# Kernel optimization log

Measured on AMD Instinct MI355X. Metric: run time of the kernel, lower is better.

Reference implementation:

```python
import jax, jax.numpy as jnp
import numpy as np

EPS = 1e-20
TEMP = 0.07
PATCH = 64
STEP = 32  # patch_size * overlap(0.5)


def zero_softmax(x, eps=1e-5):
    # ZeroSoftmax: ((exp(x)-1)^2) / (sum + eps), maps x==0 -> exactly 0 weight
    e = jnp.square(jnp.exp(x) - 1.0)
    return e / (jnp.sum(e, axis=-1, keepdims=True) + eps)


def _scaling_mask(H, W, p, step):
    # constant overlap-count mask from CRW.compute_scaling_mask (static shapes)
    sm = np.zeros((H, W), np.float32)
    for i in range(0, H - step, step):
        for j in range(0, W - step, step):
            sm[i:i + p, j:j + p] += 1.0
    return jnp.asarray(sm)


def _window_sums(m, p, step):
    # m: (B,T,SP,H,W) -> sliding-window sums (B,T,SP,nH,nW) via integral image
    ii = jnp.cumsum(jnp.cumsum(m, axis=-2), axis=-1)
    ii = jnp.pad(ii, ((0, 0), (0, 0), (0, 0), (1, 0), (1, 0)))
    H = m.shape[-2]
    nH = (H - p) // step + 1
    lo = jnp.arange(nH) * step
    hi = lo + p
    r_hi = ii[..., hi, :]   # (B,T,SP,nH,W+1)
    r_lo = ii[..., lo, :]
    return r_hi[..., hi] - r_hi[..., lo] - r_lo[..., hi] + r_lo[..., lo]


def setup_inputs() -> dict:
    key = jax.random.key(0)
    k1, k2, k3 = jax.random.split(key, 3)
    B, T, H, W = 2, 4, 256, 256
    nH = (H - PATCH) // STEP + 1  # 7
    N = nH * nH                   # 49 patches
    Cenc, D, SP = 512, 128, 64
    feats = jax.random.normal(k1, (B, N, Cenc, T), jnp.float32)
    W_head = jax.random.normal(k2, (Cenc, D), jnp.float32) / np.sqrt(Cenc)
    sp_mask = jax.random.randint(k3, (B, T, H, W), 0, SP, jnp.int32)
    return {"feats": feats, "W_head": W_head, "sp_mask": sp_mask, "max_sp_num": SP}


def reference(feats, W_head, sp_mask, max_sp_num):
    B, N, Cenc, T = feats.shape
    H, W = sp_mask.shape[-2:]
    SP = max_sp_num

    # --- pixels_to_nodes tail: projection head + L2 normalize over channel dim ---
    q = jnp.einsum('bnct,cd->bndt', feats, W_head)            # (B,N,128,T)
    nrm = jnp.maximum(jnp.linalg.norm(q, axis=2, keepdims=True), 1e-12)
    q = q / nrm
    q = jnp.transpose(q, (0, 2, 3, 1))                        # (B,128,T,N)

    # --- patches_to_sp_embeddings: windowed superpixel pooling ---
    oh = (sp_mask[:, :, None, :, :] ==
          jnp.arange(SP, dtype=sp_mask.dtype)[None, None, :, None, None]
          ).astype(jnp.float32)                               # (B,T,SP,H,W)
    sm = _scaling_mask(H, W, PATCH, STEP)                     # (H,W)
    ws = _window_sums(oh / sm, PATCH, STEP)                   # (B,T,SP,nH,nW)
    denom = jnp.sum(oh, axis=(-1, -2)) + EPS                  # (B,T,SP)
    wts = jnp.transpose(ws, (0, 1, 3, 4, 2)) / denom[:, :, None, None, :]
    wts = wts.reshape(B, T, N, SP)                            # (B,T,N,SP)
    q_sp = jnp.einsum('bdtn,btns->bdts', q, wts)              # (B,128,T,SP)

    # --- affinity + zero_softmax stochastic matrices ---
    As = jnp.einsum('bdtn,bdtm->btnm', q_sp[:, :, :-1], q_sp[:, :, 1:])  # (B,T-1,SP,SP)
    A12 = zero_softmax(As / TEMP)
    A21 = zero_softmax(jnp.swapaxes(As, -1, -2) / TEMP)

    # --- palindrome random walks + cross-entropy to cycle-consistency targets ---
    tgt = jnp.tile(jnp.arange(SP), B)
    loss = jnp.float32(0.0)
    AAs = []
    for i in range(1, T - 1):
        mats = [A12[:, k] for k in range(i + 1)] + [A21[:, k] for k in range(i, -1, -1)]
        aa = mats[0]
        for m in mats[1:]:
            aa = aa @ m
        AAs.append(aa)
        logits = jnp.log(aa + EPS).reshape(B * SP, SP)
        logp = jax.nn.log_softmax(logits, axis=-1)
        loss = loss + jnp.mean(-logp[jnp.arange(B * SP), tgt])
    return loss, jnp.stack(AAs)
```

## Files before the change

kernel.cpp:

```cpp
#include <hip/hip_runtime.h>
#include <hip/hip_bf16.h>

constexpr int NWIN = 49;
constexpr int QLD  = 52;

constexpr int OFF_WS   = 0;
constexpr int OFF_Q    = 26624;
constexpr int OFF_QSP  = 79872;
constexpr int OFF_A12  = 145408;
constexpr int OFF_A12T = 169984;
constexpr int OFF_A21  = 194560;
constexpr int OFF_A21T = 219136;

__global__ void __launch_bounds__(256, 1)
k_front(const int* __restrict__ mask, const float* __restrict__ feats,
        const float* __restrict__ Wh, float* __restrict__ ws, float* __restrict__ q) {
    if (blockIdx.x < 392) {
        int win = blockIdx.x % NWIN;
        int bt  = blockIdx.x / NWIN;
        int wy = win / 7, wx = win % 7;
        __shared__ float loc[64];
        if (threadIdx.x < 64) loc[threadIdx.x] = 0.f;
        __syncthreads();
        const int* base = mask + bt * 65536 + (wy * 32) * 256 + wx * 32;
        #pragma unroll
        for (int it = 0; it < 16; ++it) {
            int idx = it * 256 + (int)threadIdx.x;
            int r = idx >> 6, c = idx & 63;
            int s = base[r * 256 + c];
            int y = wy * 32 + r, x = wx * 32 + c;
            float w = 1.f;
            if (y >= 32 && y < 224) w *= 0.5f;
            if (x >= 32 && x < 224) w *= 0.5f;
            atomicAdd(&loc[s], w);
        }
        __syncthreads();
        if (threadIdx.x < 64) {
            ws[(bt * 64 + (int)threadIdx.x) * QLD + win] = loc[threadIdx.x];
        } else if (win == 0) {
            int s = threadIdx.x & 63;
            int col = 49 + (int)(threadIdx.x >> 6) - 1;
            ws[(bt * 64 + s) * QLD + col] = 0.f;
        }
    } else {
        int bid = blockIdx.x - 392;
        int n = bid % NWIN, b = bid / NWIN;
        __shared__ float4 f4[512];
        __shared__ float4 psum4[256];
        __shared__ float4 red4[2];
        const float4* fp4 = (const float4*)(feats + (size_t)(b * NWIN + n) * 2048);
        for (int i = threadIdx.x; i < 512; i += 256) f4[i] = fp4[i];
        __syncthreads();

        int d = threadIdx.x & 127, ch = threadIdx.x >> 7;
        float a0 = 0.f, a1 = 0.f, a2 = 0.f, a3 = 0.f;
        const float* wp = Wh + d;
        int c0 = ch * 256;
        #pragma unroll 8
        for (int c = c0; c < c0 + 256; ++c) {
            float w = wp[c * 128];
            float4 fv = f4[c];
            a0 += fv.x * w; a1 += fv.y * w; a2 += fv.z * w; a3 += fv.w * w;
        }
        psum4[threadIdx.x] = make_float4(a0, a1, a2, a3);
        __syncthreads();

        float4 A;
        if (threadIdx.x < 128) {
            float4 p0 = psum4[threadIdx.x], p1 = psum4[128 + threadIdx.x];
            A = make_float4(p0.x + p1.x, p0.y + p1.y, p0.z + p1.z, p0.w + p1.w);
            float sx = A.x * A.x, sy = A.y * A.y, sz = A.z * A.z, sw = A.w * A.w;
            for (int off = 32; off; off >>= 1) {
                sx += __shfl_down(sx, off); sy += __shfl_down(sy, off);
                sz += __shfl_down(sz, off); sw += __shfl_down(sw, off);
            }
            if ((threadIdx.x & 63) == 0) red4[threadIdx.x >> 6] = make_float4(sx, sy, sz, sw);
        }
        __syncthreads();
        if (threadIdx.x < 128) {
            float4 r0 = red4[0], r1 = red4[1];
            float ix = 1.f / fmaxf(sqrtf(r0.x + r1.x), 1e-12f);
            float iy = 1.f / fmaxf(sqrtf(r0.y + r1.y), 1e-12f);
            float iz = 1.f / fmaxf(sqrtf(r0.z + r1.z), 1e-12f);
            float iw = 1.f / fmaxf(sqrtf(r0.w + r1.w), 1e-12f);
            float* qb = q + (size_t)(b * 128 + d) * 4 * QLD + n;
            qb[0 * QLD] = A.x * ix;
            qb[1 * QLD] = A.y * iy;
            qb[2 * QLD] = A.z * iz;
            qb[3 * QLD] = A.w * iw;
        }
    }
}

__global__ void k_qsp(const float* __restrict__ q, const float* __restrict__ wsg,
                      float* __restrict__ qsp) {
    int tid = blockIdx.x * 256 + threadIdx.x;
    int s = tid & 63;
    int d = (tid >> 6) & 127;
    int t = (tid >> 13) & 3;
    int b = tid >> 15;
    const float4* qrow = (const float4*)(q + (size_t)((b * 128 + d) * 4 + t) * QLD);
    const float4* wrow = (const float4*)(wsg + (size_t)((b * 4 + t) * 64 + s) * QLD);
    float acc = 0.f, den = 0.f;
    #pragma unroll
    for (int i = 0; i < 13; ++i) {
        float4 w = wrow[i];
        float4 qv = qrow[i];
        den += w.x + w.y + w.z + w.w;
        acc += qv.x * w.x + qv.y * w.y + qv.z * w.z + qv.w * w.w;
    }
    qsp[tid] = acc / (den + 1e-20f);
}

__global__ void __launch_bounds__(256, 1)
k_as(const float* __restrict__ qsp,
     float* __restrict__ a12, float* __restrict__ a12T,
     float* __restrict__ a21, float* __restrict__ a21T, float* __restrict__ out) {
    int t = blockIdx.x % 3, b = blockIdx.x / 3;
    if (blockIdx.x == 0 && threadIdx.x == 0) out[0] = 0.f;
    __shared__ float4 qaT4[64 * 32];
    __shared__ float4 qbT4[64 * 32];
    const int tid = threadIdx.x;

    {
        const float4* gA = (const float4*)(qsp + (size_t)(b * 4 + t) * 8192);
        const float4* gB = (const float4*)(qsp + (size_t)(b * 4 + t + 1) * 8192);
        float* qaF = (float*)qaT4;
        float* qbF = (float*)qbT4;
        #pragma unroll
        for (int it = 0; it < 8; ++it) {
            int idx = it * 256 + tid;
            int d = idx >> 4, s0 = (idx & 15) << 2;
            float4 va = gA[idx];
            float4 vb = gB[idx];
            int g = d >> 2, c = d & 3;
            #pragma unroll
            for (int u = 0; u < 4; ++u) {
                int s = s0 + u;
                int w = (s * 32 + (g ^ (s & 31))) * 4 + c;
                float fa = (u == 0) ? va.x : (u == 1) ? va.y : (u == 2) ? va.z : va.w;
                float fb = (u == 0) ? vb.x : (u == 1) ? vb.y : (u == 2) ? vb.z : vb.w;
                qaF[w] = fa;
                qbF[w] = fb;
            }
        }
    }
    __syncthreads();

    const int nl = tid >> 4, ml = tid & 15;
    float acc[16];
    #pragma unroll
    for (int i = 0; i < 16; ++i) acc[i] = 0.f;
    #pragma unroll 8
    for (int k4 = 0; k4 < 32; ++k4) {
        float4 av[4], bv[4];
        #pragma unroll
        for (int i = 0; i < 4; ++i) { int n = nl + 16 * i; av[i] = qaT4[n * 32 + (k4 ^ (n & 31))]; }
        #pragma unroll
        for (int j = 0; j < 4; ++j) { int m = ml + 16 * j; bv[j] = qbT4[m * 32 + (k4 ^ (m & 31))]; }
        #pragma unroll
        for (int i = 0; i < 4; ++i)
            #pragma unroll
            for (int j = 0; j < 4; ++j)
                acc[i * 4 + j] += av[i].x * bv[j].x + av[i].y * bv[j].y
                                + av[i].z * bv[j].z + av[i].w * bv[j].w;
    }
    __syncthreads();

    float* eb = (float*)qaT4;
    float* rs = (float*)qbT4;
    float* cs = rs + 64;
    #pragma unroll
    for (int i = 0; i < 4; ++i)
        #pragma unroll
        for (int j = 0; j < 4; ++j) {
            int n = nl + 16 * i, m = ml + 16 * j;
            float x = acc[i * 4 + j] * (1.f / 0.07f);
            float e = expf(x) - 1.f;
            eb[n * 65 + m] = e * e;
        }
    __syncthreads();
    if (tid < 128) {
        int r = tid & 63; bool isrow = tid < 64;
        float a = 0.f;
        #pragma unroll
        for (int k = 0; k < 64; ++k) a += isrow ? eb[r * 65 + k] : eb[k * 65 + r];
        (isrow ? rs : cs)[r] = a + 1e-5f;
    }
    __syncthreads();
    float* p12  = a12  + (b * 3 + t) * 4096;
    float* p12T = a12T + (b * 3 + t) * 4096;
    float* p21  = a21  + (b * 3 + t) * 4096;
    float* p21T = a21T + (b * 3 + t) * 4096;
    #pragma unroll
    for (int i = 0; i < 4; ++i)
        #pragma unroll
        for (int j = 0; j < 4; ++j) {
            int n = nl + 16 * i, m = ml + 16 * j;
            float v   = eb[n * 65 + m];
            float v12 = v / rs[n];
            float v21 = v / cs[m];
            p12 [n * 64 + m] = v12;
            p12T[m * 64 + n] = v12;
            p21 [m * 64 + n] = v21;
            p21T[n * 64 + m] = v21;
        }
}


__device__ __forceinline__ void dump_mat(float* M, const float4* v) {
    #pragma unroll
    for (int it = 0; it < 4; ++it) {
        int idx = it * 256 + (int)threadIdx.x;
        int r = idx >> 4, c4 = (idx & 15) << 2;
        *(float4*)&M[r * 64 + (c4 ^ ((r & 15) << 2))] = v[it];
    }
}

__device__ __forceinline__ void mmh_sw(float* acc, const float* Ra, const float* Rb) {
    int lt = threadIdx.x & 127;
    int nl = lt >> 3, ml = lt & 7;
    int sxa = nl << 2;
    #pragma unroll
    for (int k0 = 0; k0 < 64; k0 += 4) {
        float4 av[4], bv[8];
        #pragma unroll
        for (int i = 0; i < 4; ++i)
            av[i] = *(const float4*)&Ra[(nl + 16 * i) * 64 + (k0 ^ sxa)];
        #pragma unroll
        for (int j = 0; j < 8; ++j) {
            int m = ml + 8 * j;
            bv[j] = *(const float4*)&Rb[m * 64 + (k0 ^ ((m & 15) << 2))];
        }
        #pragma unroll
        for (int i = 0; i < 4; ++i)
            #pragma unroll
            for (int j = 0; j < 8; ++j)
                acc[i * 8 + j] += av[i].x * bv[j].x + av[i].y * bv[j].y
                                + av[i].z * bv[j].z + av[i].w * bv[j].w;
    }
}

__device__ __forceinline__ void wrh_sw(float* M, const float* acc) {
    int lt = threadIdx.x & 127;
    int nl = lt >> 3, ml = lt & 7;
    #pragma unroll
    for (int i = 0; i < 4; ++i)
        #pragma unroll
        for (int j = 0; j < 8; ++j) {
            int r = nl + 16 * i, k = ml + 8 * j;
            M[r * 64 + (((k & ~3) ^ ((r & 15) << 2)) | (k & 3))] = acc[i * 8 + j];
        }
}

__device__ __forceinline__ void mm256_sw(float* acc, const float* Ra, const float* Rb) {
    int tid = threadIdx.x;
    int nl = tid >> 4, ml = tid & 15;
    int sxa = nl << 2, sxb = ml << 2;
    #pragma unroll
    for (int i = 0; i < 16; ++i) acc[i] = 0.f;
    #pragma unroll 4
    for (int k0 = 0; k0 < 64; k0 += 4) {
        float4 av[4], bv[4];
        #pragma unroll
        for (int i = 0; i < 4; ++i)
            av[i] = *(const float4*)&Ra[(nl + 16 * i) * 64 + (k0 ^ sxa)];
        #pragma unroll
        for (int j = 0; j < 4; ++j)
            bv[j] = *(const float4*)&Rb[(ml + 16 * j) * 64 + (k0 ^ sxb)];
        #pragma unroll
        for (int i = 0; i < 4; ++i)
            #pragma unroll
            for (int j = 0; j < 4; ++j)
                acc[i * 4 + j] += av[i].x * bv[j].x + av[i].y * bv[j].y
                                + av[i].z * bv[j].z + av[i].w * bv[j].w;
    }
}

__device__ __forceinline__ void store_loss(const float* acc, float* __restrict__ aa,
                                           float* __restrict__ out, float* red) {
    int tid = threadIdx.x;
    int nl = tid >> 4, ml = tid & 15;
    #pragma unroll
    for (int i = 0; i < 4; ++i)
        #pragma unroll
        for (int j = 0; j < 4; ++j)
            aa[(nl + 16 * i) * 64 + (ml + 16 * j)] = acc[i * 4 + j];
    int l = tid & 63;
    float part = 0.f;
    #pragma unroll
    for (int i = 0; i < 4; ++i) {
        float rsum = acc[i * 4 + 0] + acc[i * 4 + 1] + acc[i * 4 + 2] + acc[i * 4 + 3];
        rsum += __shfl_down(rsum, 8, 16);
        rsum += __shfl_down(rsum, 4, 16);
        rsum += __shfl_down(rsum, 2, 16);
        rsum += __shfl_down(rsum, 1, 16);
        float dv = __shfl(acc[5 * i], (l & 48) | nl, 64);
        if ((l & 15) == 0) part += logf(rsum + 6.4e-19f) - logf(dv + 1e-20f);
    }
    for (int off = 32; off; off >>= 1) part += __shfl_down(part, off);
    if (l == 0) red[tid >> 6] = part;
    __syncthreads();
    if (tid == 0) atomicAdd(out, (red[0] + red[1] + red[2] + red[3]) * (1.f / 128.f));
}

__global__ void __launch_bounds__(256, 1)
k_chain(const float* __restrict__ a12, const float* __restrict__ a12T,
        const float* __restrict__ a21, const float* __restrict__ a21T,
        float* __restrict__ out) {
    int path = blockIdx.x & 1, b = blockIdx.x >> 1;
    __shared__ float M[4 * 4096];
    float* M0 = M;
    float* M1 = M + 4096;
    float* M2 = M + 8192;
    float* M3 = M + 12288;
    const int tid = threadIdx.x;

    const float4* L0 = (const float4*)(a12  + (b * 3 + 0) * 4096);
    const float4* L1 = (const float4*)(a12T + (b * 3 + 1) * 4096);
    const float4* L2 = (const float4*)(a21T + (b * 3 + 0) * 4096);
    const float4* L3 = (const float4*)(a21  + (b * 3 + 1) * 4096);
    const float4* L4 = (const float4*)(a12T + (b * 3 + 2) * 4096);
    const float4* L5 = (const float4*)(a21  + (b * 3 + 2) * 4096);

    float4 pf[6][4];
    #pragma unroll
    for (int it = 0; it < 4; ++it) {
        int idx = it * 256 + tid;
        pf[0][it] = L0[idx];
        pf[1][it] = L1[idx];
        pf[2][it] = L2[idx];
        pf[3][it] = L3[idx];
    }
    if (path) {
        #pragma unroll
        for (int it = 0; it < 4; ++it) {
            int idx = it * 256 + tid;
            pf[4][it] = L4[idx];
            pf[5][it] = L5[idx];
        }
    }
    dump_mat(M0, pf[0]);
    dump_mat(M1, pf[1]);
    dump_mat(M2, pf[2]);
    dump_mat(M3, pf[3]);
    __syncthreads();

    int half = tid >> 7;
    float hacc[32];
    #pragma unroll
    for (int i = 0; i < 32; ++i) hacc[i] = 0.f;
    mmh_sw(hacc, half ? M2 : M0, half ? M3 : M1);
    __syncthreads();
    wrh_sw(half ? M3 : M1, hacc);
    if (path) { dump_mat(M0, pf[4]); dump_mat(M2, pf[5]); }
    __syncthreads();

    if (path == 0) {
        float acc[16];
        mm256_sw(acc, M1, M3);
        store_loss(acc, out + 1 + b * 4096, out, M0);
    } else {
        float hacc2[32];
        #pragma unroll
        for (int i = 0; i < 32; ++i) hacc2[i] = 0.f;
        mmh_sw(hacc2, half ? M3 : M1, half ? M2 : M0);
        __syncthreads();
        wrh_sw(half ? M1 : M0, hacc2);
        __syncthreads();
        float acc[16];
        mm256_sw(acc, M0, M1);
        store_loss(acc, out + 1 + (2 + b) * 4096, out, M2);
    }
}

extern "C" void kernel_launch(void* const* d_in, const int* in_sizes, int n_in,
                              void* d_out, int out_size, void* d_ws, size_t ws_size,
                              hipStream_t stream) {
    const float* feats = (const float*)d_in[0];
    const float* Wh    = (const float*)d_in[1];
    const int*   mask  = (const int*)d_in[2];
    float* out = (float*)d_out;
    float* ws  = (float*)d_ws;

    float* ws_sums = ws + OFF_WS;
    float* q       = ws + OFF_Q;
    float* qsp     = ws + OFF_QSP;
    float* a12     = ws + OFF_A12;
    float* a12T    = ws + OFF_A12T;
    float* a21     = ws + OFF_A21;
    float* a21T    = ws + OFF_A21T;

    k_front<<<392 + 2 * NWIN, 256, 0, stream>>>(mask, feats, Wh, ws_sums, q);
    k_qsp<<<256, 256, 0, stream>>>(q, ws_sums, qsp);
    k_as<<<6, 256, 0, stream>>>(qsp, a12, a12T, a21, a21T, out);
    k_chain<<<4, 256, 0, stream>>>(a12, a12T, a21, a21T, out);
}
```

Before: 118.9 us.

## Fuse affinity and chain kernels into one persistent kernel with grid barriers

```diff
diff --git a/kernel.cpp b/kernel.cpp
--- a/kernel.cpp
+++ b/kernel.cpp
@@ -11,6 +11,11 @@
 constexpr int OFF_A12T = 169984;
 constexpr int OFF_A21  = 194560;
 constexpr int OFF_A21T = 219136;
+constexpr int OFF_P    = 243712;
+constexpr int OFF_R1T  = 251904;
+constexpr int OFF_L    = 260096;
+constexpr int OFF_RT   = 268288;
+constexpr int OFF_BAR  = 276480;
 
 __global__ void __launch_bounds__(256, 1)
 k_front(const int* __restrict__ mask, const float* __restrict__ feats,
@@ -93,7 +98,12 @@
 }
 
 __global__ void k_qsp(const float* __restrict__ q, const float* __restrict__ wsg,
-                      float* __restrict__ qsp) {
+                      float* __restrict__ qsp, float* __restrict__ out,
+                      int* __restrict__ bar) {
+    if (blockIdx.x == 0 && threadIdx.x < 4) {
+        bar[threadIdx.x] = 0;
+        if (threadIdx.x == 0) out[0] = 0.f;
+    }
     int tid = blockIdx.x * 256 + threadIdx.x;
     int s = tid & 63;
     int d = (tid >> 6) & 127;
@@ -112,101 +122,6 @@
     qsp[tid] = acc / (den + 1e-20f);
 }
 
-__global__ void __launch_bounds__(256, 1)
-k_as(const float* __restrict__ qsp,
-     float* __restrict__ a12, float* __restrict__ a12T,
-     float* __restrict__ a21, float* __restrict__ a21T, float* __restrict__ out) {
-    int t = blockIdx.x % 3, b = blockIdx.x / 3;
-    if (blockIdx.x == 0 && threadIdx.x == 0) out[0] = 0.f;
-    __shared__ float4 qaT4[64 * 32];
-    __shared__ float4 qbT4[64 * 32];
-    const int tid = threadIdx.x;
-
-    {
-        const float4* gA = (const float4*)(qsp + (size_t)(b * 4 + t) * 8192);
-        const float4* gB = (const float4*)(qsp + (size_t)(b * 4 + t + 1) * 8192);
-        float* qaF = (float*)qaT4;
-        float* qbF = (float*)qbT4;
-        #pragma unroll
-        for (int it = 0; it < 8; ++it) {
-            int idx = it * 256 + tid;
-            int d = idx >> 4, s0 = (idx & 15) << 2;
-            float4 va = gA[idx];
-            float4 vb = gB[idx];
-            int g = d >> 2, c = d & 3;
-            #pragma unroll
-            for (int u = 0; u < 4; ++u) {
-                int s = s0 + u;
-                int w = (s * 32 + (g ^ (s & 31))) * 4 + c;
-                float fa = (u == 0) ? va.x : (u == 1) ? va.y : (u == 2) ? va.z : va.w;
-                float fb = (u == 0) ? vb.x : (u == 1) ? vb.y : (u == 2) ? vb.z : vb.w;
-                qaF[w] = fa;
-                qbF[w] = fb;
-            }
-        }
-    }
-    __syncthreads();
-
-    const int nl = tid >> 4, ml = tid & 15;
-    float acc[16];
-    #pragma unroll
-    for (int i = 0; i < 16; ++i) acc[i] = 0.f;
-    #pragma unroll 8
-    for (int k4 = 0; k4 < 32; ++k4) {
-        float4 av[4], bv[4];
-        #pragma unroll
-        for (int i = 0; i < 4; ++i) { int n = nl + 16 * i; av[i] = qaT4[n * 32 + (k4 ^ (n & 31))]; }
-        #pragma unroll
-        for (int j = 0; j < 4; ++j) { int m = ml + 16 * j; bv[j] = qbT4[m * 32 + (k4 ^ (m & 31))]; }
-        #pragma unroll
-        for (int i = 0; i < 4; ++i)
-            #pragma unroll
-            for (int j = 0; j < 4; ++j)
-                acc[i * 4 + j] += av[i].x * bv[j].x + av[i].y * bv[j].y
-                                + av[i].z * bv[j].z + av[i].w * bv[j].w;
-    }
-    __syncthreads();
-
-    float* eb = (float*)qaT4;
-    float* rs = (float*)qbT4;
-    float* cs = rs + 64;
-    #pragma unroll
-    for (int i = 0; i < 4; ++i)
-        #pragma unroll
-        for (int j = 0; j < 4; ++j) {
-            int n = nl + 16 * i, m = ml + 16 * j;
-            float x = acc[i * 4 + j] * (1.f / 0.07f);
-            float e = expf(x) - 1.f;
-            eb[n * 65 + m] = e * e;
-        }
-    __syncthreads();
-    if (tid < 128) {
-        int r = tid & 63; bool isrow = tid < 64;
-        float a = 0.f;
-        #pragma unroll
-        for (int k = 0; k < 64; ++k) a += isrow ? eb[r * 65 + k] : eb[k * 65 + r];
-        (isrow ? rs : cs)[r] = a + 1e-5f;
-    }
-    __syncthreads();
-    float* p12  = a12  + (b * 3 + t) * 4096;
-    float* p12T = a12T + (b * 3 + t) * 4096;
-    float* p21  = a21  + (b * 3 + t) * 4096;
-    float* p21T = a21T + (b * 3 + t) * 4096;
-    #pragma unroll
-    for (int i = 0; i < 4; ++i)
-        #pragma unroll
-        for (int j = 0; j < 4; ++j) {
-            int n = nl + 16 * i, m = ml + 16 * j;
-            float v   = eb[n * 65 + m];
-            float v12 = v / rs[n];
-            float v21 = v / cs[m];
-            p12 [n * 64 + m] = v12;
-            p12T[m * 64 + n] = v12;
-            p21 [m * 64 + n] = v21;
-            p21T[n * 64 + m] = v21;
-        }
-}
-
 
 __device__ __forceinline__ void dump_mat(float* M, const float4* v) {
     #pragma unroll
@@ -217,40 +132,20 @@
     }
 }
 
-__device__ __forceinline__ void mmh_sw(float* acc, const float* Ra, const float* Rb) {
-    int lt = threadIdx.x & 127;
-    int nl = lt >> 3, ml = lt & 7;
-    int sxa = nl << 2;
-    #pragma unroll
-    for (int k0 = 0; k0 < 64; k0 += 4) {
-        float4 av[4], bv[8];
-        #pragma unroll
-        for (int i = 0; i < 4; ++i)
-            av[i] = *(const float4*)&Ra[(nl + 16 * i) * 64 + (k0 ^ sxa)];
-        #pragma unroll
-        for (int j = 0; j < 8; ++j) {
-            int m = ml + 8 * j;
-            bv[j] = *(const float4*)&Rb[m * 64 + (k0 ^ ((m & 15) << 2))];
-        }
-        #pragma unroll
-        for (int i = 0; i < 4; ++i)
-            #pragma unroll
-            for (int j = 0; j < 8; ++j)
-                acc[i * 8 + j] += av[i].x * bv[j].x + av[i].y * bv[j].y
-                                + av[i].z * bv[j].z + av[i].w * bv[j].w;
-    }
-}
-
-__device__ __forceinline__ void wrh_sw(float* M, const float* acc) {
-    int lt = threadIdx.x & 127;
-    int nl = lt >> 3, ml = lt & 7;
-    #pragma unroll
-    for (int i = 0; i < 4; ++i)
-        #pragma unroll
-        for (int j = 0; j < 8; ++j) {
-            int r = nl + 16 * i, k = ml + 8 * j;
-            M[r * 64 + (((k & ~3) ^ ((r & 15) << 2)) | (k & 3))] = acc[i * 8 + j];
-        }
+__device__ __forceinline__ void stage2(float* Ma, float* Mb,
+                                       const float* __restrict__ Ga,
+                                       const float* __restrict__ Gb) {
+    const float4* ga = (const float4*)Ga;
+    const float4* gb = (const float4*)Gb;
+    float4 va[4], vb[4];
+    #pragma unroll
+    for (int it = 0; it < 4; ++it) {
+        int idx = it * 256 + (int)threadIdx.x;
+        va[it] = ga[idx];
+        vb[it] = gb[idx];
+    }
+    dump_mat(Ma, va);
+    dump_mat(Mb, vb);
 }
 
 __device__ __forceinline__ void mm256_sw(float* acc, const float* Ra, const float* Rb) {
@@ -275,6 +170,15 @@
                 acc[i * 4 + j] += av[i].x * bv[j].x + av[i].y * bv[j].y
                                 + av[i].z * bv[j].z + av[i].w * bv[j].w;
     }
+}
+
+__device__ __forceinline__ void store_mat(float* __restrict__ G, const float* acc) {
+    int nl = threadIdx.x >> 4, ml = threadIdx.x & 15;
+    #pragma unroll
+    for (int i = 0; i < 4; ++i)
+        #pragma unroll
+        for (int j = 0; j < 4; ++j)
+            G[(nl + 16 * i) * 64 + ml + 16 * j] = acc[i * 4 + j];
 }
 
 __device__ __forceinline__ void store_loss(const float* acc, float* __restrict__ aa,
@@ -304,73 +208,174 @@
     if (tid == 0) atomicAdd(out, (red[0] + red[1] + red[2] + red[3]) * (1.f / 128.f));
 }
 
+__device__ __forceinline__ void gbar(int* cnt, int target) {
+    __threadfence();
+    __syncthreads();
+    if (threadIdx.x == 0) {
+        __hip_atomic_fetch_add(cnt, 1, __ATOMIC_ACQ_REL, __HIP_MEMORY_SCOPE_AGENT);
+        while (__hip_atomic_load(cnt, __ATOMIC_ACQUIRE, __HIP_MEMORY_SCOPE_AGENT) < target)
+            __builtin_amdgcn_s_sleep(2);
+    }
+    __syncthreads();
+    __threadfence();
+}
+
 __global__ void __launch_bounds__(256, 1)
-k_chain(const float* __restrict__ a12, const float* __restrict__ a12T,
-        const float* __restrict__ a21, const float* __restrict__ a21T,
-        float* __restrict__ out) {
-    int path = blockIdx.x & 1, b = blockIdx.x >> 1;
-    __shared__ float M[4 * 4096];
-    float* M0 = M;
-    float* M1 = M + 4096;
-    float* M2 = M + 8192;
-    float* M3 = M + 12288;
+k_tail(const float* __restrict__ qsp,
+       float* __restrict__ a12, float* __restrict__ a12T,
+       float* __restrict__ a21, float* __restrict__ a21T,
+       float* __restrict__ wsP, float* __restrict__ wsR1T,
+       float* __restrict__ wsL, float* __restrict__ wsRT,
+       float* __restrict__ out, int* __restrict__ bar) {
+    __shared__ float SM[16384];
     const int tid = threadIdx.x;
-
-    const float4* L0 = (const float4*)(a12  + (b * 3 + 0) * 4096);
-    const float4* L1 = (const float4*)(a12T + (b * 3 + 1) * 4096);
-    const float4* L2 = (const float4*)(a21T + (b * 3 + 0) * 4096);
-    const float4* L3 = (const float4*)(a21  + (b * 3 + 1) * 4096);
-    const float4* L4 = (const float4*)(a12T + (b * 3 + 2) * 4096);
-    const float4* L5 = (const float4*)(a21  + (b * 3 + 2) * 4096);
-
-    float4 pf[6][4];
-    #pragma unroll
-    for (int it = 0; it < 4; ++it) {
-        int idx = it * 256 + tid;
-        pf[0][it] = L0[idx];
-        pf[1][it] = L1[idx];
-        pf[2][it] = L2[idx];
-        pf[3][it] = L3[idx];
-    }
-    if (path) {
-        #pragma unroll
-        for (int it = 0; it < 4; ++it) {
-            int idx = it * 256 + tid;
-            pf[4][it] = L4[idx];
-            pf[5][it] = L5[idx];
-        }
-    }
-    dump_mat(M0, pf[0]);
-    dump_mat(M1, pf[1]);
-    dump_mat(M2, pf[2]);
-    dump_mat(M3, pf[3]);
-    __syncthreads();
-
-    int half = tid >> 7;
-    float hacc[32];
-    #pragma unroll
-    for (int i = 0; i < 32; ++i) hacc[i] = 0.f;
-    mmh_sw(hacc, half ? M2 : M0, half ? M3 : M1);
-    __syncthreads();
-    wrh_sw(half ? M3 : M1, hacc);
-    if (path) { dump_mat(M0, pf[4]); dump_mat(M2, pf[5]); }
-    __syncthreads();
-
-    if (path == 0) {
+    const int blk = blockIdx.x;
+
+    {
+        int t = blk % 3, b = blk / 3;
+        float4* qaT4 = (float4*)SM;
+        float4* qbT4 = (float4*)SM + 2048;
+        {
+            const float4* gA = (const float4*)(qsp + (size_t)(b * 4 + t) * 8192);
+            const float4* gB = (const float4*)(qsp + (size_t)(b * 4 + t + 1) * 8192);
+            float* qaF = (float*)qaT4;
+            float* qbF = (float*)qbT4;
+            #pragma unroll
+            for (int it = 0; it < 8; ++it) {
+                int idx = it * 256 + tid;
+                int d = idx >> 4, s0 = (idx & 15) << 2;
+                float4 va = gA[idx];
+                float4 vb = gB[idx];
+                int g = d >> 2, c = d & 3;
+                #pragma unroll
+                for (int u = 0; u < 4; ++u) {
+                    int s = s0 + u;
+                    int w = (s * 32 + (g ^ (s & 31))) * 4 + c;
+                    float fa = (u == 0) ? va.x : (u == 1) ? va.y : (u == 2) ? va.z : va.w;
+                    float fb = (u == 0) ? vb.x : (u == 1) ? vb.y : (u == 2) ? vb.z : vb.w;
+                    qaF[w] = fa;
+                    qbF[w] = fb;
+                }
+            }
+        }
+        __syncthreads();
+
+        const int nl = tid >> 4, ml = tid & 15;
         float acc[16];
-        mm256_sw(acc, M1, M3);
-        store_loss(acc, out + 1 + b * 4096, out, M0);
-    } else {
-        float hacc2[32];
-        #pragma unroll
-        for (int i = 0; i < 32; ++i) hacc2[i] = 0.f;
-        mmh_sw(hacc2, half ? M3 : M1, half ? M2 : M0);
-        __syncthreads();
-        wrh_sw(half ? M1 : M0, hacc2);
+        #pragma unroll
+        for (int i = 0; i < 16; ++i) acc[i] = 0.f;
+        #pragma unroll 8
+        for (int k4 = 0; k4 < 32; ++k4) {
+            float4 av[4], bv[4];
+            #pragma unroll
+            for (int i = 0; i < 4; ++i) { int n = nl + 16 * i; av[i] = qaT4[n * 32 + (k4 ^ (n & 31))]; }
+            #pragma unroll
+            for (int j = 0; j < 4; ++j) { int m = ml + 16 * j; bv[j] = qbT4[m * 32 + (k4 ^ (m & 31))]; }
+            #pragma unroll
+            for (int i = 0; i < 4; ++i)
+                #pragma unroll
+                for (int j = 0; j < 4; ++j)
+                    acc[i * 4 + j] += av[i].x * bv[j].x + av[i].y * bv[j].y
+                                    + av[i].z * bv[j].z + av[i].w * bv[j].w;
+        }
+        __syncthreads();
+
+        float* eb = (float*)qaT4;
+        float* rs = (float*)qbT4;
+        float* cs = rs + 64;
+        #pragma unroll
+        for (int i = 0; i < 4; ++i)
+            #pragma unroll
+            for (int j = 0; j < 4; ++j) {
+                int n = nl + 16 * i, m = ml + 16 * j;
+                float x = acc[i * 4 + j] * (1.f / 0.07f);
+                float e = expf(x) - 1.f;
+                eb[n * 65 + m] = e * e;
+            }
+        __syncthreads();
+        if (tid < 128) {
+            int r = tid & 63; bool isrow = tid < 64;
+            float a = 0.f;
+            #pragma unroll
+            for (int k = 0; k < 64; ++k) a += isrow ? eb[r * 65 + k] : eb[k * 65 + r];
+            (isrow ? rs : cs)[r] = a + 1e-5f;
+        }
+        __syncthreads();
+        float* p12  = a12  + (b * 3 + t) * 4096;
+        float* p12T = a12T + (b * 3 + t) * 4096;
+        float* p21  = a21  + (b * 3 + t) * 4096;
+        float* p21T = a21T + (b * 3 + t) * 4096;
+        #pragma unroll
+        for (int i = 0; i < 4; ++i)
+            #pragma unroll
+            for (int j = 0; j < 4; ++j) {
+                int n = nl + 16 * i, m = ml + 16 * j;
+                float v   = eb[n * 65 + m];
+                float v12 = v / rs[n];
+                float v21 = v / cs[m];
+                if (t == 0) {
+                    p12 [n * 64 + m] = v12;
+                    p21T[n * 64 + m] = v21;
+                } else {
+                    p12T[m * 64 + n] = v12;
+                    p21 [m * 64 + n] = v21;
+                }
+            }
+    }
+    gbar(bar + 0, 6);
+
+    if (blk < 4) {
+        int b = blk >> 1, which = blk & 1;
+        float* Ma = SM;
+        float* Mb = SM + 4096;
+        if (which == 0) stage2(Ma, Mb, a12  + (b * 3 + 0) * 4096, a12T + (b * 3 + 1) * 4096);
+        else            stage2(Ma, Mb, a21T + (b * 3 + 0) * 4096, a21  + (b * 3 + 1) * 4096);
         __syncthreads();
         float acc[16];
-        mm256_sw(acc, M0, M1);
-        store_loss(acc, out + 1 + (2 + b) * 4096, out, M2);
+        mm256_sw(acc, Ma, Mb);
+        store_mat((which == 0 ? wsP : wsR1T) + b * 4096, acc);
+    }
+    gbar(bar + 1, 6);
+
+    {
+        float* Ma = SM;
+        float* Mb = SM + 4096;
+        float* red = SM + 8192;
+        if (blk < 2) {
+            int b = blk;
+            stage2(Ma, Mb, wsP + b * 4096, wsR1T + b * 4096);
+            __syncthreads();
+            float acc[16];
+            mm256_sw(acc, Ma, Mb);
+            store_loss(acc, out + 1 + b * 4096, out, red);
+        } else if (blk < 4) {
+            int b = blk - 2;
+            stage2(Ma, Mb, wsP + b * 4096, a12T + (b * 3 + 2) * 4096);
+            __syncthreads();
+            float acc[16];
+            mm256_sw(acc, Ma, Mb);
+            store_mat(wsL + b * 4096, acc);
+        } else {
+            int b = blk - 4;
+            stage2(Ma, Mb, wsR1T + b * 4096, a21 + (b * 3 + 2) * 4096);
+            __syncthreads();
+            float acc[16];
+            mm256_sw(acc, Ma, Mb);
+            store_mat(wsRT + b * 4096, acc);
+        }
+    }
+    gbar(bar + 2, 6);
+
+    if (blk < 2) {
+        int b = blk;
+        float* Ma = SM;
+        float* Mb = SM + 4096;
+        float* red = SM + 8192;
+        stage2(Ma, Mb, wsL + b * 4096, wsRT + b * 4096);
+        __syncthreads();
+        float acc[16];
+        mm256_sw(acc, Ma, Mb);
+        store_loss(acc, out + 1 + (2 + b) * 4096, out, red);
     }
 }
 
@@ -390,9 +395,14 @@
     float* a12T    = ws + OFF_A12T;
     float* a21     = ws + OFF_A21;
     float* a21T    = ws + OFF_A21T;
+    float* wsP     = ws + OFF_P;
+    float* wsR1T   = ws + OFF_R1T;
+    float* wsL     = ws + OFF_L;
+    float* wsRT    = ws + OFF_RT;
+    int*   bar     = (int*)(ws + OFF_BAR);
 
     k_front<<<392 + 2 * NWIN, 256, 0, stream>>>(mask, feats, Wh, ws_sums, q);
-    k_qsp<<<256, 256, 0, stream>>>(q, ws_sums, qsp);
-    k_as<<<6, 256, 0, stream>>>(qsp, a12, a12T, a21, a21T, out);
-    k_chain<<<4, 256, 0, stream>>>(a12, a12T, a21, a21T, out);
-}
+    k_qsp<<<256, 256, 0, stream>>>(q, ws_sums, qsp, out, bar);
+    k_tail<<<6, 256, 0, stream>>>(qsp, a12, a12T, a21, a21T,
+                                  wsP, wsR1T, wsL, wsRT, out, bar);
+}
```

Result: faster. 114.8 us (-3.4%).
